# Optimization experiments

Hardware: AMD Instinct MI355X
Metric: run time of the kernel (lower is better)

## Reference

```python
import jax, jax.numpy as jnp
import numpy as np

B, F, C, D = 4, 60082, 14695, 256
KN, KH = 64, 128


def _leaky(x):
    return jnp.where(x >= 0, x, 0.01 * x)  # nn.LeakyReLU default slope


def setup_inputs() -> dict:
    key = jax.random.key(0)
    ks = jax.random.split(key, 20)
    d = {}
    d["company_emb"] = jax.random.normal(ks[0], (B, D), jnp.float32)
    d["field_emb"] = jax.random.normal(ks[1], (F, D), jnp.float32)
    d["raw_field_embed"] = jax.random.normal(ks[2], (F, D), jnp.float32)
    d["comp_table"] = jax.random.normal(ks[3], (C, D), jnp.float32)
    d["field_table"] = jax.random.normal(ks[4], (F, D), jnp.float32)
    d["W_proj"] = jax.random.normal(ks[5], (D, D), jnp.float32) / np.sqrt(D)
    d["b_proj"] = jnp.zeros((D,), jnp.float32)
    d["theta"] = jax.random.uniform(ks[6], (C, 1), jnp.float32)
    d["alpha_fields"] = jax.random.uniform(ks[7], (F, 1), jnp.float32)
    d["w_ff"] = jax.random.normal(ks[8], (D,), jnp.float32) / np.sqrt(D)
    d["b_ff"] = jnp.zeros((), jnp.float32)
    d["w_fc"] = jax.random.normal(ks[9], (D,), jnp.float32) / np.sqrt(D)
    d["b_fc"] = jnp.zeros((), jnp.float32)
    d["W1"] = jax.random.normal(ks[10], (D, D // 2), jnp.float32) / np.sqrt(D)
    d["b1"] = jnp.zeros((D // 2,), jnp.float32)
    d["W2"] = jax.random.normal(ks[11], (D // 2, D), jnp.float32) / np.sqrt(D // 2)
    d["b2"] = jnp.zeros((D,), jnp.float32)
    d["now_nodes"] = jax.random.randint(ks[12], (B, KN), 0, F, dtype=jnp.int32)
    d["his_nodes"] = jax.random.randint(ks[13], (B, KH), 0, F, dtype=jnp.int32)
    d["com_id"] = jax.random.randint(ks[14], (B,), 0, C, dtype=jnp.int32)
    return d


def reference(company_emb, field_emb, raw_field_embed, comp_table, field_table,
              W_proj, b_proj, theta, alpha_fields, w_ff, b_ff, w_fc, b_fc,
              W1, b1, W2, b2, now_nodes, his_nodes, com_id):
    # company memory/static mix: (B, D)
    th = theta[com_id]  # (B, 1)
    company_mem = (1.0 - th) * company_emb + th * comp_table[com_id]
    # (dropout is identity in eval mode)

    # shared projected field table: (F, D)
    embed_base = field_table @ W_proj + b_proj

    bidx = jnp.arange(B)[:, None]
    # beta mask: 1 at now + his indices per batch element
    beta = (jnp.zeros((B, F), jnp.float32)
            .at[bidx, now_nodes].set(1.0)
            .at[bidx, his_nodes].set(1.0))
    alpha = alpha_fields[:, 0]  # (F,)

    # (B, F, D) scaled base embedding
    embed = (1.0 - beta * alpha[None, :])[..., None] * embed_base[None]

    # now-node additive update (gather-then-set, matching torch advanced assignment)
    now_proj = field_emb[now_nodes]  # (B, KN, D)
    embed = embed.at[bidx, now_nodes].set(
        embed[bidx, now_nodes] + alpha_fields[now_nodes] * now_proj)

    # his-node MLP update: Linear -> LeakyReLU -> Linear on raw field memory
    h = _leaky(raw_field_embed[his_nodes] @ W1 + b1) @ W2 + b2  # (B, KH, D)
    embed = embed.at[bidx, his_nodes].set(
        embed[bidx, his_nodes] + alpha_fields[his_nodes] * h)

    fields_out = embed @ w_ff + b_ff        # (B, F)
    company_out = company_mem @ w_fc + b_fc  # (B,)
    return fields_out + company_out[:, None]
```

## Files before the change

kernel.cpp:

```cpp
#include <hip/hip_runtime.h>

#define Dc 256
#define Bc 4
#define Fc 60082
#define KNc 64
#define KHc 128


__device__ __forceinline__ float wave_reduce_sum(float v) {
    #pragma unroll
    for (int off = 32; off > 0; off >>= 1)
        v += __shfl_down(v, off, 64);
    return v;
}

__global__ void k_pre(const float* __restrict__ company_emb,
                      const float* __restrict__ comp_table,
                      const float* __restrict__ W_proj,
                      const float* __restrict__ b_proj,
                      const float* __restrict__ theta,
                      const float* __restrict__ w_ff,
                      const float* __restrict__ b_ff,
                      const float* __restrict__ w_fc,
                      const float* __restrict__ b_fc,
                      const float* __restrict__ W2,
                      const float* __restrict__ b2,
                      const int* __restrict__ com_id,
                      float* __restrict__ ws)
{
    int t = threadIdx.x;
    float* u      = ws;
    float* v2     = ws + 256;
    float* constb = ws + 384;
    float* scal   = ws + 388;

    {
        float acc = 0.f;
        const float* row = W_proj + t * Dc;
        #pragma unroll 4
        for (int i = 0; i < Dc; ++i) acc += row[i] * w_ff[i];
        u[t] = acc;
    }
    if (t < 128) {
        float acc = 0.f;
        const float* row = W2 + t * Dc;
        #pragma unroll 4
        for (int i = 0; i < Dc; ++i) acc += row[i] * w_ff[i];
        v2[t] = acc;
    }
    if (t == 0) {
        float c2 = 0.f, c0 = 0.f;
        for (int i = 0; i < Dc; ++i) { c2 += b2[i] * w_ff[i]; c0 += b_proj[i] * w_ff[i]; }
        scal[0] = c2;
        scal[1] = c0;
    }
    if (t < Bc) {
        int cid = com_id[t];
        float th = theta[cid];
        const float* ce = company_emb + t * Dc;
        const float* ct = comp_table + (size_t)cid * Dc;
        float acc = 0.f;
        for (int i = 0; i < Dc; ++i)
            acc += ((1.f - th) * ce[i] + th * ct[i]) * w_fc[i];
        constb[t] = acc + b_fc[0] + b_ff[0];
    }
}

__global__ void k_s(const float* __restrict__ field_table,
                    const float* __restrict__ ws_u,
                    const float* __restrict__ ws_scal,
                    float* __restrict__ s)
{
    int w = (blockIdx.x * blockDim.x + threadIdx.x) >> 6;
    int lane = threadIdx.x & 63;
    if (w >= Fc) return;
    const float4* row = (const float4*)(field_table + (size_t)w * Dc);
    const float4* uu  = (const float4*)ws_u;
    float4 a = row[lane];
    float4 b = uu[lane];
    float acc = a.x*b.x + a.y*b.y + a.z*b.z + a.w*b.w;
    acc = wave_reduce_sum(acc);
    if (lane == 0) s[w] = acc + ws_scal[1];
}

__global__ void k_bcast(const float* __restrict__ s,
                        const float* __restrict__ constb,
                        float* __restrict__ out)
{
    int i = blockIdx.x * blockDim.x + threadIdx.x;
    if (i >= Bc * Fc) return;
    int b = i / Fc;
    int f = i - b * Fc;
    out[i] = s[f] + constb[b];
}

__global__ void k_fix(const float* __restrict__ field_emb,
                      const float* __restrict__ raw_field_embed,
                      const float* __restrict__ alpha_fields,
                      const float* __restrict__ w_ff,
                      const float* __restrict__ W1,
                      const float* __restrict__ b1,
                      const float* __restrict__ ws,
                      const float* __restrict__ s,
                      const int* __restrict__ now_nodes,
                      const int* __restrict__ his_nodes,
                      float* __restrict__ out)
{
    const float* v2     = ws + 256;
    const float* constb = ws + 384;
    const float* scal   = ws + 388;

    const int NPB = KNc + KHc;
    int gw = (blockIdx.x * blockDim.x + threadIdx.x) >> 6;
    int lane = threadIdx.x & 63;
    if (gw >= Bc * NPB) return;
    int b = gw / NPB;
    int k = gw - b * NPB;
    int f = (k < KNc) ? now_nodes[b * KNc + k]
                      : his_nodes[b * KHc + (k - KNc)];

    int nn = now_nodes[b * KNc + lane];
    bool in_now = __any(nn == f);
    int h0 = his_nodes[b * KHc + lane];
    int h1 = his_nodes[b * KHc + 64 + lane];
    bool in_his = __any((h0 == f) || (h1 == f));

    float alpha = alpha_fields[f];
    float val = (1.f - alpha) * s[f] + constb[b];

    if (in_now) {
        const float4* row = (const float4*)(field_emb + (size_t)f * Dc);
        const float4* w   = (const float4*)w_ff;
        float4 a = row[lane];
        float4 ww = w[lane];
        float acc = a.x*ww.x + a.y*ww.y + a.z*ww.z + a.w*ww.w;
        acc = wave_reduce_sum(acc);
        acc = __shfl(acc, 0, 64);
        val += alpha * acc;
    }
    if (in_his) {
        float acc0 = 0.f, acc1 = 0.f;
        const float* raw = raw_field_embed + (size_t)f * Dc;
        #pragma unroll 4
        for (int d = 0; d < Dc; ++d) {
            float r = raw[d];
            acc0 += r * W1[d * 128 + lane];
            acc1 += r * W1[d * 128 + 64 + lane];
        }
        float g0 = acc0 + b1[lane];
        float g1 = acc1 + b1[64 + lane];
        g0 = (g0 >= 0.f) ? g0 : 0.01f * g0;
        g1 = (g1 >= 0.f) ? g1 : 0.01f * g1;
        float p = g0 * v2[lane] + g1 * v2[64 + lane];
        p = wave_reduce_sum(p);
        p = __shfl(p, 0, 64);
        val += alpha * (p + scal[0]);
    }
    if (lane == 0) out[(size_t)b * Fc + f] = val;
}

extern "C" void kernel_launch(void* const* d_in, const int* in_sizes, int n_in,
                              void* d_out, int out_size, void* d_ws, size_t ws_size,
                              hipStream_t stream) {
    const float* company_emb     = (const float*)d_in[0];
    const float* field_emb       = (const float*)d_in[1];
    const float* raw_field_embed = (const float*)d_in[2];
    const float* comp_table      = (const float*)d_in[3];
    const float* field_table     = (const float*)d_in[4];
    const float* W_proj          = (const float*)d_in[5];
    const float* b_proj          = (const float*)d_in[6];
    const float* theta           = (const float*)d_in[7];
    const float* alpha_fields    = (const float*)d_in[8];
    const float* w_ff            = (const float*)d_in[9];
    const float* b_ff            = (const float*)d_in[10];
    const float* w_fc            = (const float*)d_in[11];
    const float* b_fc            = (const float*)d_in[12];
    const float* W1              = (const float*)d_in[13];
    const float* b1              = (const float*)d_in[14];
    const float* W2              = (const float*)d_in[15];
    const float* b2              = (const float*)d_in[16];
    const int*   now_nodes       = (const int*)d_in[17];
    const int*   his_nodes       = (const int*)d_in[18];
    const int*   com_id          = (const int*)d_in[19];

    float* ws = (float*)d_ws;
    float* s  = ws + 512;
    float* out = (float*)d_out;

    k_pre<<<1, 256, 0, stream>>>(company_emb, comp_table, W_proj, b_proj, theta,
                                 w_ff, b_ff, w_fc, b_fc, W2, b2, com_id, ws);

    int s_blocks = (Fc + 3) / 4;
    k_s<<<s_blocks, 256, 0, stream>>>(field_table, ws, ws + 388, s);

    int bc_blocks = (Bc * Fc + 255) / 256;
    k_bcast<<<bc_blocks, 256, 0, stream>>>(s, ws + 384, out);

    int fix_blocks = (Bc * (KNc + KHc)) / 4;
    k_fix<<<fix_blocks, 256, 0, stream>>>(field_emb, raw_field_embed, alpha_fields,
                                          w_ff, W1, b1, ws, s,
                                          now_nodes, his_nodes, out);
}
```

Measured before the change: 271.7 us.

## Parallelize precompute across waves and fuse broadcast into row-dot kernel

The single-block serial precompute kernel becomes a multi-block kernel where each wave computes one 256-length dot product with float4 loads and a butterfly reduction. The separate broadcast kernel is folded into the field-table dot kernel: each wave now handles four rows and writes all four batch outputs directly, which removes one launch and a reread of the intermediate vector. The history MLP loop uses float4 loads of the raw row. The butterfly reduction leaves the sum in every lane, so the extra shuffles are dropped.

```diff
diff --git a/kernel.cpp b/kernel.cpp
--- a/kernel.cpp
+++ b/kernel.cpp
@@ -7,10 +7,10 @@
 #define KHc 128
 
 
-__device__ __forceinline__ float wave_reduce_sum(float v) {
+__device__ __forceinline__ float wave_reduce_sum_bfly(float v) {
     #pragma unroll
     for (int off = 32; off > 0; off >>= 1)
-        v += __shfl_down(v, off, 64);
+        v += __shfl_xor(v, off, 64);
     return v;
 }
 
@@ -28,70 +28,100 @@
                       const int* __restrict__ com_id,
                       float* __restrict__ ws)
 {
-    int t = threadIdx.x;
-    float* u      = ws;
-    float* v2     = ws + 256;
-    float* constb = ws + 384;
-    float* scal   = ws + 388;
-
-    {
-        float acc = 0.f;
-        const float* row = W_proj + t * Dc;
-        #pragma unroll 4
-        for (int i = 0; i < Dc; ++i) acc += row[i] * w_ff[i];
-        u[t] = acc;
-    }
-    if (t < 128) {
-        float acc = 0.f;
-        const float* row = W2 + t * Dc;
-        #pragma unroll 4
-        for (int i = 0; i < Dc; ++i) acc += row[i] * w_ff[i];
-        v2[t] = acc;
-    }
-    if (t == 0) {
-        float c2 = 0.f, c0 = 0.f;
-        for (int i = 0; i < Dc; ++i) { c2 += b2[i] * w_ff[i]; c0 += b_proj[i] * w_ff[i]; }
-        scal[0] = c2;
-        scal[1] = c0;
-    }
-    if (t < Bc) {
-        int cid = com_id[t];
+    int gw = (blockIdx.x * blockDim.x + threadIdx.x) >> 6;
+    int lane = threadIdx.x & 63;
+    if (gw >= 390) return;
+
+    const float4* wf4 = (const float4*)w_ff;
+    float val = 0.f;
+    float addend = 0.f;
+    float* dst;
+
+    if (gw < 256) {
+        float4 a = ((const float4*)(W_proj + (size_t)gw * Dc))[lane];
+        float4 b = wf4[lane];
+        val = a.x*b.x + a.y*b.y + a.z*b.z + a.w*b.w;
+        dst = ws + gw;
+    } else if (gw < 384) {
+        int j = gw - 256;
+        float4 a = ((const float4*)(W2 + (size_t)j * Dc))[lane];
+        float4 b = wf4[lane];
+        val = a.x*b.x + a.y*b.y + a.z*b.z + a.w*b.w;
+        dst = ws + 256 + j;
+    } else if (gw < 388) {
+        int b_ = gw - 384;
+        int cid = com_id[b_];
         float th = theta[cid];
-        const float* ce = company_emb + t * Dc;
-        const float* ct = comp_table + (size_t)cid * Dc;
-        float acc = 0.f;
-        for (int i = 0; i < Dc; ++i)
-            acc += ((1.f - th) * ce[i] + th * ct[i]) * w_fc[i];
-        constb[t] = acc + b_fc[0] + b_ff[0];
-    }
-}
-
+        float4 x = ((const float4*)(company_emb + (size_t)b_ * Dc))[lane];
+        float4 y = ((const float4*)(comp_table + (size_t)cid * Dc))[lane];
+        float4 w = ((const float4*)w_fc)[lane];
+        float4 m;
+        m.x = (1.f - th) * x.x + th * y.x;
+        m.y = (1.f - th) * x.y + th * y.y;
+        m.z = (1.f - th) * x.z + th * y.z;
+        m.w = (1.f - th) * x.w + th * y.w;
+        val = m.x*w.x + m.y*w.y + m.z*w.z + m.w*w.w;
+        addend = b_fc[0] + b_ff[0];
+        dst = ws + 384 + b_;
+    } else if (gw == 388) {
+        float4 a = ((const float4*)b2)[lane];
+        float4 b = wf4[lane];
+        val = a.x*b.x + a.y*b.y + a.z*b.z + a.w*b.w;
+        dst = ws + 388;
+    } else {
+        float4 a = ((const float4*)b_proj)[lane];
+        float4 b = wf4[lane];
+        val = a.x*b.x + a.y*b.y + a.z*b.z + a.w*b.w;
+        dst = ws + 389;
+    }
+    val = wave_reduce_sum_bfly(val);
+    if (lane == 0) *dst = val + addend;
+}
+
+#define RPW 4
 __global__ void k_s(const float* __restrict__ field_table,
-                    const float* __restrict__ ws_u,
-                    const float* __restrict__ ws_scal,
-                    float* __restrict__ s)
+                    const float* __restrict__ ws,
+                    float* __restrict__ s,
+                    float* __restrict__ out)
 {
-    int w = (blockIdx.x * blockDim.x + threadIdx.x) >> 6;
+    int gw = (blockIdx.x * blockDim.x + threadIdx.x) >> 6;
     int lane = threadIdx.x & 63;
-    if (w >= Fc) return;
-    const float4* row = (const float4*)(field_table + (size_t)w * Dc);
-    const float4* uu  = (const float4*)ws_u;
-    float4 a = row[lane];
-    float4 b = uu[lane];
-    float acc = a.x*b.x + a.y*b.y + a.z*b.z + a.w*b.w;
-    acc = wave_reduce_sum(acc);
-    if (lane == 0) s[w] = acc + ws_scal[1];
-}
-
-__global__ void k_bcast(const float* __restrict__ s,
-                        const float* __restrict__ constb,
-                        float* __restrict__ out)
-{
-    int i = blockIdx.x * blockDim.x + threadIdx.x;
-    if (i >= Bc * Fc) return;
-    int b = i / Fc;
-    int f = i - b * Fc;
-    out[i] = s[f] + constb[b];
+    int f0 = gw * RPW;
+    if (f0 >= Fc) return;
+
+    float4 b = ((const float4*)ws)[lane];
+    float c0 = ws[389];
+
+    float acc[RPW];
+    #pragma unroll
+    for (int r = 0; r < RPW; ++r) {
+        int f = f0 + r;
+        float4 a = make_float4(0.f, 0.f, 0.f, 0.f);
+        if (f < Fc) a = ((const float4*)(field_table + (size_t)f * Dc))[lane];
+        acc[r] = a.x*b.x + a.y*b.y + a.z*b.z + a.w*b.w;
+    }
+    #pragma unroll
+    for (int r = 0; r < RPW; ++r)
+        acc[r] = wave_reduce_sum_bfly(acc[r]);
+
+    auto pick = [&](int i) {
+        float v = acc[0];
+        v = (i == 1) ? acc[1] : v;
+        v = (i == 2) ? acc[2] : v;
+        v = (i == 3) ? acc[3] : v;
+        return v;
+    };
+
+    if (lane < 16) {
+        int r  = lane & 3;
+        int bb = lane >> 2;
+        int f  = f0 + r;
+        if (f < Fc) out[(size_t)bb * Fc + f] = pick(r) + c0 + ws[384 + bb];
+    } else if (lane >= 60) {
+        int r = lane - 60;
+        int f = f0 + r;
+        if (f < Fc) s[f] = pick(r) + c0;
+    }
 }
 
 __global__ void k_fix(const float* __restrict__ field_emb,
@@ -129,31 +159,30 @@
     float val = (1.f - alpha) * s[f] + constb[b];
 
     if (in_now) {
-        const float4* row = (const float4*)(field_emb + (size_t)f * Dc);
-        const float4* w   = (const float4*)w_ff;
-        float4 a = row[lane];
-        float4 ww = w[lane];
+        float4 a  = ((const float4*)(field_emb + (size_t)f * Dc))[lane];
+        float4 ww = ((const float4*)w_ff)[lane];
         float acc = a.x*ww.x + a.y*ww.y + a.z*ww.z + a.w*ww.w;
-        acc = wave_reduce_sum(acc);
-        acc = __shfl(acc, 0, 64);
+        acc = wave_reduce_sum_bfly(acc);
         val += alpha * acc;
     }
     if (in_his) {
         float acc0 = 0.f, acc1 = 0.f;
-        const float* raw = raw_field_embed + (size_t)f * Dc;
-        #pragma unroll 4
-        for (int d = 0; d < Dc; ++d) {
-            float r = raw[d];
-            acc0 += r * W1[d * 128 + lane];
-            acc1 += r * W1[d * 128 + 64 + lane];
+        const float4* raw4 = (const float4*)(raw_field_embed + (size_t)f * Dc);
+        #pragma unroll 2
+        for (int d4 = 0; d4 < Dc / 4; ++d4) {
+            float4 r4 = raw4[d4];
+            const float* base = W1 + d4 * 4 * 128;
+            acc0 += r4.x * base[lane]       + r4.y * base[128 + lane]
+                  + r4.z * base[256 + lane] + r4.w * base[384 + lane];
+            acc1 += r4.x * base[64 + lane]      + r4.y * base[128 + 64 + lane]
+                  + r4.z * base[256 + 64 + lane] + r4.w * base[384 + 64 + lane];
         }
         float g0 = acc0 + b1[lane];
         float g1 = acc1 + b1[64 + lane];
         g0 = (g0 >= 0.f) ? g0 : 0.01f * g0;
         g1 = (g1 >= 0.f) ? g1 : 0.01f * g1;
         float p = g0 * v2[lane] + g1 * v2[64 + lane];
-        p = wave_reduce_sum(p);
-        p = __shfl(p, 0, 64);
+        p = wave_reduce_sum_bfly(p);
         val += alpha * (p + scal[0]);
     }
     if (lane == 0) out[(size_t)b * Fc + f] = val;
@@ -183,18 +212,16 @@
     const int*   his_nodes       = (const int*)d_in[18];
     const int*   com_id          = (const int*)d_in[19];
 
-    float* ws = (float*)d_ws;
-    float* s  = ws + 512;
+    float* ws  = (float*)d_ws;
+    float* s   = ws + 512;
     float* out = (float*)d_out;
 
-    k_pre<<<1, 256, 0, stream>>>(company_emb, comp_table, W_proj, b_proj, theta,
-                                 w_ff, b_ff, w_fc, b_fc, W2, b2, com_id, ws);
-
-    int s_blocks = (Fc + 3) / 4;
-    k_s<<<s_blocks, 256, 0, stream>>>(field_table, ws, ws + 388, s);
-
-    int bc_blocks = (Bc * Fc + 255) / 256;
-    k_bcast<<<bc_blocks, 256, 0, stream>>>(s, ws + 384, out);
+    k_pre<<<(390 + 3) / 4, 256, 0, stream>>>(company_emb, comp_table, W_proj, b_proj,
+                                             theta, w_ff, b_ff, w_fc, b_fc, W2, b2,
+                                             com_id, ws);
+
+    int waves = (Fc + RPW - 1) / RPW;
+    k_s<<<(waves + 3) / 4, 256, 0, stream>>>(field_table, ws, s, out);
 
     int fix_blocks = (Bc * (KNc + KHc)) / 4;
     k_fix<<<fix_blocks, 256, 0, stream>>>(field_emb, raw_field_embed, alpha_fields,
```

Measured after the change: 230.6 us. 1.18x faster.
